# Performance work log

Hardware: AMD Instinct MI355X
Metric: run time of the kernel (lower is better)

## Reference

```python
import jax, jax.numpy as jnp
import numpy as np

N = 50000      # nodes
E = 800000     # edges
CIN = 128
CH = 128
COUT = 64
EPS = 1e-5     # BatchNorm eps


def setup_inputs() -> dict:
    key = jax.random.key(0)
    ks = jax.random.split(key, 16)
    s = 0.1  # weight scale for numerical stability
    return {
        "x": jax.random.normal(ks[0], (N, CIN), jnp.float32),
        "edge_index": jax.random.randint(ks[1], (2, E), 0, N, jnp.int32),
        "edge_weights": jax.random.uniform(ks[2], (E,), jnp.float32),
        "w1": jax.random.normal(ks[3], (CIN, CH), jnp.float32) * s,
        "b1": jnp.zeros((CH,), jnp.float32),
        "bn1_g": jnp.ones((CH,), jnp.float32),
        "bn1_b": jnp.zeros((CH,), jnp.float32),
        "bn1_m": jax.random.normal(ks[4], (CH,), jnp.float32) * 0.1,
        "bn1_v": jax.random.uniform(ks[5], (CH,), jnp.float32) + 0.5,
        "conv_ws": jax.random.normal(ks[6], (2, CH, CH), jnp.float32) * s,
        "conv_bs": jnp.zeros((2, CH), jnp.float32),
        "bns_g": jnp.ones((2, CH), jnp.float32),
        "bns_b": jnp.zeros((2, CH), jnp.float32),
        "bns_m": jax.random.normal(ks[7], (2, CH), jnp.float32) * 0.1,
        "bns_v": jax.random.uniform(ks[8], (2, CH), jnp.float32) + 0.5,
        "lin1_w": jax.random.normal(ks[9], (CH, CH), jnp.float32) * s,
        "lin1_b": jnp.zeros((CH,), jnp.float32),
        "lin2_w": jax.random.normal(ks[10], (CH, COUT), jnp.float32) * s,
        "lin2_b": jnp.zeros((COUT,), jnp.float32),
    }


def _bn(h, g, b, m, v):
    # BatchNorm1d in eval mode: running statistics
    return (h - m) * jax.lax.rsqrt(v + EPS) * g + b


def _gcn(h, w, b, src, dst, norm, n):
    # GCNConv: out[dst] += norm_e * (h @ W)[src]  (self loops already in src/dst)
    h = h @ w
    msg = h[src] * norm[:, None]                 # [E+N, CH]
    return jax.ops.segment_sum(msg, dst, num_segments=n) + b


def reference(x, edge_index, edge_weights, w1, b1, bn1_g, bn1_b, bn1_m, bn1_v,
              conv_ws, conv_bs, bns_g, bns_b, bns_m, bns_v,
              lin1_w, lin1_b, lin2_w, lin2_b):
    n = x.shape[0]
    loop = jnp.arange(n, dtype=edge_index.dtype)
    src = jnp.concatenate([edge_index[0], loop])
    dst = jnp.concatenate([edge_index[1], loop])
    ew = jnp.concatenate([edge_weights, jnp.ones((n,), edge_weights.dtype)])
    # symmetric degree normalization (PyG gcn_norm)
    deg = jax.ops.segment_sum(ew, dst, num_segments=n)
    dis = jnp.where(deg > 0, jax.lax.rsqrt(deg), 0.0)
    norm = dis[src] * ew * dis[dst]

    lrelu = jax.nn.leaky_relu  # slope 0.01, matches F.leaky_relu default
    h = lrelu(_bn(_gcn(x, w1, b1, src, dst, norm, n), bn1_g, bn1_b, bn1_m, bn1_v))
    for i in range(conv_ws.shape[0]):
        h = lrelu(_bn(_gcn(h, conv_ws[i], conv_bs[i], src, dst, norm, n),
                      bns_g[i], bns_b[i], bns_m[i], bns_v[i]) + h)
    h = lrelu(h @ lin1_w + lin1_b)
    # dropout is identity in eval mode
    return h @ lin2_w + lin2_b
```

## Files before the change

kernel.cpp:

```cpp
#include <hip/hip_runtime.h>
#include <hip/hip_bf16.h>


constexpr int   NN    = 50000;
constexpr int   EE    = 800000;
constexpr int   CH    = 128;
constexpr int   SLOTS = 64;
constexpr int   NBUK  = 782;
constexpr int   RCAP  = 2048;
constexpr int   EPB   = 2048;
constexpr float EPS   = 1e-5f;

typedef __attribute__((ext_vector_type(8))) short bf16x8;
typedef __attribute__((ext_vector_type(4))) float f32x4;
typedef unsigned long long u64;
typedef unsigned short u16;

__device__ inline u16 f2bf_rne(float f) {
  unsigned u = __float_as_uint(f);
  unsigned r = u + 0x7fffu + ((u >> 16) & 1u);
  return (u16)(r >> 16);
}
__device__ inline float bf2f(unsigned h16) {
  return __uint_as_float(h16 << 16);
}


__global__ __launch_bounds__(256) void bin_kernel(const int* __restrict__ ei,
                                                  const float* __restrict__ ew,
                                                  unsigned* __restrict__ gcur,
                                                  u64* __restrict__ bins) {
  __shared__ unsigned cnt[NBUK];
  __shared__ unsigned base[NBUK];
  const int tid = threadIdx.x;
  for (int b = tid; b < NBUK; b += 256) cnt[b] = 0;
  __syncthreads();
  const int e0 = blockIdx.x * EPB;
  unsigned pk[8]; u16 bkt[8]; u16 rnk[8]; unsigned char dl[8];
  #pragma unroll
  for (int i = 0; i < 8; i++) {
    int e = e0 + i * 256 + tid;
    if (e < EE) {
      int s = ei[e], d = ei[EE + e];
      float w = ew[e];
      bkt[i] = (u16)(d >> 6);
      dl[i]  = (unsigned char)(d & 63);
      pk[i]  = ((unsigned)f2bf_rne(w) << 16) | (unsigned)s;
      rnk[i] = (u16)atomicAdd(&cnt[bkt[i]], 1u);
    } else bkt[i] = 0xffffu;
  }
  __syncthreads();
  for (int b = tid; b < NBUK; b += 256) {
    unsigned c = cnt[b];
    base[b] = c ? atomicAdd(&gcur[b * 16], c) : 0u;
  }
  __syncthreads();
  #pragma unroll
  for (int i = 0; i < 8; i++) {
    if (bkt[i] == 0xffffu) continue;
    unsigned pos = base[bkt[i]] + rnk[i];
    if (pos < RCAP)
      bins[(size_t)bkt[i] * RCAP + pos] = ((u64)dl[i] << 32) | pk[i];
  }
}


__global__ __launch_bounds__(256) void scatter_kernel(const unsigned* __restrict__ gcur,
                                                      const u64* __restrict__ bins,
                                                      unsigned* __restrict__ ell,
                                                      float* __restrict__ dis) {
  __shared__ unsigned rank[64];
  __shared__ float    wsum[64];
  const int b   = blockIdx.x;
  const int tid = threadIdx.x;
  if (tid < 64) { rank[tid] = 1u; wsum[tid] = 0.f; }
  __syncthreads();
  unsigned cnt = gcur[b * 16];
  if (cnt > RCAP) cnt = RCAP;
  const u64* src = bins + (size_t)b * RCAP;
  for (unsigned i = tid; i < cnt; i += 256) {
    u64 v = src[i];
    unsigned pk = (unsigned)v;
    unsigned dl = (unsigned)(v >> 32);
    unsigned r = atomicAdd(&rank[dl], 1u);
    if (r < SLOTS)
      ell[((size_t)(b * 64 + dl)) * SLOTS + r] = pk;
    atomicAdd(&wsum[dl], bf2f(pk >> 16));
  }
  __syncthreads();
  if (tid < 64) {
    int node = b * 64 + tid;
    if (node < NN) {
      unsigned c = rank[tid];
      if (c > SLOTS) c = SLOTS;
      ell[(size_t)node * SLOTS] = c;
      dis[node] = rsqrtf(1.0f + wsum[tid]);
    }
  }
}

constexpr int NB_WZ = (73728 + 384 + 255) / 256;

__global__ void wswz_kernel(
    const float* __restrict__ w1, const float* __restrict__ bn1_g, const float* __restrict__ bn1_v,
    const float* __restrict__ conv_ws, const float* __restrict__ bns_g, const float* __restrict__ bns_v,
    const float* __restrict__ lin1_w, const float* __restrict__ lin2_w,
    const float* __restrict__ b1, const float* __restrict__ bn1_b, const float* __restrict__ bn1_m,
    const float* __restrict__ conv_bs, const float* __restrict__ bns_b, const float* __restrict__ bns_m,
    u16* __restrict__ w1h, u16* __restrict__ w1l,
    u16* __restrict__ c0h, u16* __restrict__ c0l,
    u16* __restrict__ c1h, u16* __restrict__ c1l,
    u16* __restrict__ l1h, u16* __restrict__ l1l,
    u16* __restrict__ l2h, u16* __restrict__ l2l,
    float* __restrict__ beff)
{
  int idx = blockIdx.x * 256 + threadIdx.x;
  if (idx >= 73728) {
    int r = idx - 73728;
    if (r >= 384) return;
    int l = r >> 7, c = r & 127;
    float bc, gg, bb, mm, vv;
    if (l == 0) { bc = b1[c]; gg = bn1_g[c]; bb = bn1_b[c]; mm = bn1_m[c]; vv = bn1_v[c]; }
    else {
      int o = (l - 1) * 128 + c;
      bc = conv_bs[o]; gg = bns_g[o]; bb = bns_b[o]; mm = bns_m[o]; vv = bns_v[o];
    }
    beff[r] = (bc - mm) * gg * rsqrtf(vv + EPS) + bb;
    return;
  }
  const float* W; const float* g = nullptr; const float* v = nullptr;
  u16 *hi, *lo; int CO = 128; int local;
  if      (idx < 16384) { W = w1;              g = bn1_g;     v = bn1_v;     hi = w1h; lo = w1l; local = idx; }
  else if (idx < 32768) { W = conv_ws;         g = bns_g;     v = bns_v;     hi = c0h; lo = c0l; local = idx - 16384; }
  else if (idx < 49152) { W = conv_ws + 16384; g = bns_g+128; v = bns_v+128; hi = c1h; lo = c1l; local = idx - 32768; }
  else if (idx < 65536) { W = lin1_w;                                        hi = l1h; lo = l1l; local = idx - 49152; }
  else                  { W = lin2_w;                                        hi = l2h; lo = l2l; local = idx - 65536; CO = 64; }
  int k = local / CO, n = local % CO;
  float w = W[local];
  if (g) w *= g[n] * rsqrtf(v[n] + EPS);
  int NCT = CO / 16;
  int kchunk = k >> 5, kin = k & 31, quad = kin >> 3, j = kin & 7;
  int ct = n >> 4, l = (quad << 4) | (n & 15);
  size_t pos = ((size_t)(kchunk * NCT + ct) * 64 + l) * 8 + j;
  u16 h = f2bf_rne(w);
  hi[pos] = h;
  lo[pos] = f2bf_rne(w - bf2f(h));
}

__global__ __launch_bounds__(256) void gemm1_kernel(
    const float* __restrict__ Ain,
    const u16* __restrict__ Whi, const u16* __restrict__ Wlo,
    const float* __restrict__ dis, u16* __restrict__ Cout)
{
  __shared__ float lds[64][CH + 4];
  const int tid  = threadIdx.x;
  const int wave = tid >> 6;
  const int lane = tid & 63;
  const int quad = lane >> 4;
  const int mrow = lane & 15;
  const int row0 = blockIdx.x * 64;

  int arow = row0 + wave * 16 + mrow;
  if (arow >= NN) arow = NN - 1;

  bf16x8 ahi[4], alo[4];
  const float* Ar = Ain + (size_t)arow * CH;
  #pragma unroll
  for (int c = 0; c < 4; c++) {
    int off = c * 32 + quad * 8;
    float4 f0 = *(const float4*)(Ar + off);
    float4 f1 = *(const float4*)(Ar + off + 4);
    float f[8] = {f0.x, f0.y, f0.z, f0.w, f1.x, f1.y, f1.z, f1.w};
    #pragma unroll
    for (int j = 0; j < 8; j++) {
      u16 h = f2bf_rne(f[j]);
      ahi[c][j] = (short)h;
      alo[c][j] = (short)f2bf_rne(f[j] - bf2f(h));
    }
  }

  f32x4 acc[8];
  #pragma unroll
  for (int t = 0; t < 8; t++) acc[t] = (f32x4){0.f, 0.f, 0.f, 0.f};
  #pragma unroll
  for (int c = 0; c < 4; c++) {
    #pragma unroll
    for (int t = 0; t < 8; t++) {
      size_t base = ((size_t)(c * 8 + t) * 64 + lane) * 8;
      bf16x8 bh = *(const bf16x8*)(Whi + base);
      bf16x8 bl = *(const bf16x8*)(Wlo + base);
      acc[t] = __builtin_amdgcn_mfma_f32_16x16x32_bf16(ahi[c], bh, acc[t], 0, 0, 0);
      acc[t] = __builtin_amdgcn_mfma_f32_16x16x32_bf16(alo[c], bh, acc[t], 0, 0, 0);
      acc[t] = __builtin_amdgcn_mfma_f32_16x16x32_bf16(ahi[c], bl, acc[t], 0, 0, 0);
    }
  }

  #pragma unroll
  for (int t = 0; t < 8; t++)
    #pragma unroll
    for (int r = 0; r < 4; r++)
      lds[wave * 16 + quad * 4 + r][t * 16 + mrow] = acc[t][r];
  __syncthreads();

  #pragma unroll
  for (int i = tid; i < 64 * CH / 4; i += 256) {
    int row = (i * 4) / CH;
    int col = (i * 4) % CH;
    int grow = row0 + row;
    if (grow >= NN) continue;
    float rs = dis[grow];
    const float* lp = &lds[row][col];
    u16* cp = (u16*)Cout + (size_t)grow * CH + col;
    unsigned p0 = ((unsigned)f2bf_rne(lp[1] * rs) << 16) | f2bf_rne(lp[0] * rs);
    unsigned p1 = ((unsigned)f2bf_rne(lp[3] * rs) << 16) | f2bf_rne(lp[2] * rs);
    *(uint2*)cp = make_uint2(p0, p1);
  }
}

template<bool RES, bool WH>
__device__ __forceinline__ void gather4_pipe(
    const u16* __restrict__ hwin, const unsigned* __restrict__ ell,
    const float* __restrict__ dis, const float* __restrict__ beff,
    const u16* __restrict__ res, u16* __restrict__ hout,
    unsigned* __restrict__ hsrow,
    int nbase, int lane, int sub, int grp)
{
  auto ndof = [&](int r) { int n = nbase + r; return n < NN ? n : NN - 1; };

  unsigned wcur  = ell[(size_t)ndof(0) * SLOTS + lane];
  unsigned wnext = ell[(size_t)ndof(1) * SLOTS + lane];

  int r = 0, j = 0;
  int cnt = __shfl((int)wcur, 0); if (cnt > SLOTS) cnt = SLOTS;

  float a[8] = {0.f, 0.f, 0.f, 0.f, 0.f, 0.f, 0.f, 0.f};

  unsigned sA[4]; float wA[4]; uint4 hA[4];

  {
    int nd0 = ndof(0);
    #pragma unroll
    for (int q = 0; q < 4; q++) {
      int jj = q * 4 + grp;
      unsigned e = (unsigned)__shfl((int)wcur, jj);
      float wv = (jj == 0) ? 1.0f : bf2f(e >> 16);
      unsigned s = (jj == 0) ? (unsigned)nd0 : (e & 0xffffu);
      if (jj >= cnt) { wv = 0.f; s = (unsigned)nd0; }
      sA[q] = s; wA[q] = wv;
    }
    #pragma unroll
    for (int q = 0; q < 4; q++)
      hA[q] = *(const uint4*)(hwin + (size_t)sA[q] * CH + sub * 8);
  }

  while (true) {
    int jn = j + 16, rn = r;
    const bool cross = (jn >= cnt);
    if (cross) { rn = r + 1; jn = 0; }
    const bool havenext = (rn < 4);

    unsigned sB[4]; float wB[4]; uint4 hB[4];
    int cntN = cnt;
    if (havenext) {
      unsigned wsel = cross ? wnext : wcur;
      if (cross) { cntN = __shfl((int)wnext, 0); if (cntN > SLOTS) cntN = SLOTS; }
      int ndn = ndof(rn);
      #pragma unroll
      for (int q = 0; q < 4; q++) {
        int jj = jn + q * 4 + grp;
        unsigned e = (unsigned)__shfl((int)wsel, jj & 63);
        float wv = (jj == 0) ? 1.0f : bf2f(e >> 16);
        unsigned s = (jj == 0) ? (unsigned)ndn : (e & 0xffffu);
        if (jj >= cntN) { wv = 0.f; s = (unsigned)ndn; }
        sB[q] = s; wB[q] = wv;
      }
      #pragma unroll
      for (int q = 0; q < 4; q++)
        hB[q] = *(const uint4*)(hwin + (size_t)sB[q] * CH + sub * 8);
    }

    #pragma unroll
    for (int q = 0; q < 4; q++) {
      float w = wA[q];
      a[0] = fmaf(w, bf2f(hA[q].x & 0xffffu), a[0]); a[1] = fmaf(w, bf2f(hA[q].x >> 16), a[1]);
      a[2] = fmaf(w, bf2f(hA[q].y & 0xffffu), a[2]); a[3] = fmaf(w, bf2f(hA[q].y >> 16), a[3]);
      a[4] = fmaf(w, bf2f(hA[q].z & 0xffffu), a[4]); a[5] = fmaf(w, bf2f(hA[q].z >> 16), a[5]);
      a[6] = fmaf(w, bf2f(hA[q].w & 0xffffu), a[6]); a[7] = fmaf(w, bf2f(hA[q].w >> 16), a[7]);
    }

    if (cross) {
      #pragma unroll
      for (int k = 0; k < 8; k++) {
        a[k] += __shfl_xor(a[k], 16);
        a[k] += __shfl_xor(a[k], 32);
      }
      int nd = ndof(r), node = nbase + r;
      if (grp == 0) {
        float disd = dis[nd];
        int c = sub * 8;
        float4 be0 = *(const float4*)(beff + c);
        float4 be1 = *(const float4*)(beff + c + 4);
        float y[8];
        y[0] = a[0] * disd + be0.x; y[1] = a[1] * disd + be0.y;
        y[2] = a[2] * disd + be0.z; y[3] = a[3] * disd + be0.w;
        y[4] = a[4] * disd + be1.x; y[5] = a[5] * disd + be1.y;
        y[6] = a[6] * disd + be1.z; y[7] = a[7] * disd + be1.w;
        if constexpr (RES) {
          uint4 rr = *(const uint4*)(res + (size_t)nd * CH + c);
          y[0] += bf2f(rr.x & 0xffffu); y[1] += bf2f(rr.x >> 16);
          y[2] += bf2f(rr.y & 0xffffu); y[3] += bf2f(rr.y >> 16);
          y[4] += bf2f(rr.z & 0xffffu); y[5] += bf2f(rr.z >> 16);
          y[6] += bf2f(rr.w & 0xffffu); y[7] += bf2f(rr.w >> 16);
        }
        #pragma unroll
        for (int k = 0; k < 8; k++) y[k] = y[k] > 0.f ? y[k] : 0.01f * y[k];
        uint4 o;
        o.x = ((unsigned)f2bf_rne(y[1]) << 16) | f2bf_rne(y[0]);
        o.y = ((unsigned)f2bf_rne(y[3]) << 16) | f2bf_rne(y[2]);
        o.z = ((unsigned)f2bf_rne(y[5]) << 16) | f2bf_rne(y[4]);
        o.w = ((unsigned)f2bf_rne(y[7]) << 16) | f2bf_rne(y[6]);
        if constexpr (WH) {
          if (node < NN) *(uint4*)(hout + (size_t)node * CH + c) = o;
        }
        *(uint4*)&hsrow[r * 68 + sub * 4] = o;
      }
      #pragma unroll
      for (int k = 0; k < 8; k++) a[k] = 0.f;
      wcur = wnext;
      if (r + 2 < 4) wnext = ell[(size_t)ndof(r + 2) * SLOTS + lane];
      if (havenext) cnt = cntN;
    }

    if (!havenext) break;
    r = rn; j = jn;
    #pragma unroll
    for (int q = 0; q < 4; q++) { sA[q] = sB[q]; wA[q] = wB[q]; hA[q] = hB[q]; }
  }
}

template<bool RES>
__global__ __launch_bounds__(256, 6) void fuse_kernel(
    const u16* __restrict__ hwin,
    const unsigned* __restrict__ ell, const float* __restrict__ dis,
    const float* __restrict__ beff, const u16* __restrict__ res,
    const u16* __restrict__ Whi, const u16* __restrict__ Wlo,
    u16* __restrict__ hout, u16* __restrict__ hwout)
{
  __shared__ unsigned hs[16][68];
  const int tid  = threadIdx.x;
  const int wave = tid >> 6;
  const int lane = tid & 63;
  const int sub  = lane & 15;
  const int grp  = lane >> 4;
  const int row0 = blockIdx.x * 16;

  gather4_pipe<RES, true>(hwin, ell, dis, beff, res, hout,
                          &hs[wave * 4][0], row0 + wave * 4, lane, sub, grp);
  __syncthreads();

  bf16x8 af[4];
  #pragma unroll
  for (int c = 0; c < 4; c++)
    af[c] = *(const bf16x8*)&hs[sub][c * 16 + grp * 4];

  f32x4 acc[2];
  #pragma unroll
  for (int t = 0; t < 2; t++) acc[t] = (f32x4){0.f, 0.f, 0.f, 0.f};
  #pragma unroll
  for (int c = 0; c < 4; c++) {
    #pragma unroll
    for (int t = 0; t < 2; t++) {
      size_t base = ((size_t)(c * 8 + wave * 2 + t) * 64 + lane) * 8;
      bf16x8 bh = *(const bf16x8*)(Whi + base);
      bf16x8 bl = *(const bf16x8*)(Wlo + base);
      acc[t] = __builtin_amdgcn_mfma_f32_16x16x32_bf16(af[c], bh, acc[t], 0, 0, 0);
      acc[t] = __builtin_amdgcn_mfma_f32_16x16x32_bf16(af[c], bl, acc[t], 0, 0, 0);
    }
  }

  #pragma unroll
  for (int r = 0; r < 4; r++) {
    int grow = row0 + grp * 4 + r;
    if (grow >= NN) continue;
    float rs = dis[grow];
    #pragma unroll
    for (int t = 0; t < 2; t++)
      hwout[(size_t)grow * CH + wave * 32 + t * 16 + sub] = f2bf_rne(acc[t][r] * rs);
  }
}

__global__ __launch_bounds__(256, 6) void fuse_last_kernel(
    const u16* __restrict__ hwin,
    const unsigned* __restrict__ ell, const float* __restrict__ dis,
    const float* __restrict__ beff, const u16* __restrict__ res,
    const u16* __restrict__ l1h, const u16* __restrict__ l1l,
    const float* __restrict__ b1,
    const u16* __restrict__ l2h, const u16* __restrict__ l2l,
    const float* __restrict__ b2, float* __restrict__ out)
{
  __shared__ unsigned hs[16][68];
  __shared__ float    fs[16][132];
  const int tid  = threadIdx.x;
  const int wave = tid >> 6;
  const int lane = tid & 63;
  const int sub  = lane & 15;
  const int grp  = lane >> 4;
  const int row0 = blockIdx.x * 16;

  gather4_pipe<true, false>(hwin, ell, dis, beff, res, nullptr,
                            &hs[wave * 4][0], row0 + wave * 4, lane, sub, grp);
  __syncthreads();

  bf16x8 af[4];
  #pragma unroll
  for (int c = 0; c < 4; c++)
    af[c] = *(const bf16x8*)&hs[sub][c * 16 + grp * 4];

  f32x4 acc[2];
  #pragma unroll
  for (int t = 0; t < 2; t++) acc[t] = (f32x4){0.f, 0.f, 0.f, 0.f};
  #pragma unroll
  for (int c = 0; c < 4; c++) {
    #pragma unroll
    for (int t = 0; t < 2; t++) {
      size_t base = ((size_t)(c * 8 + wave * 2 + t) * 64 + lane) * 8;
      bf16x8 bh = *(const bf16x8*)(l1h + base);
      bf16x8 bl = *(const bf16x8*)(l1l + base);
      acc[t] = __builtin_amdgcn_mfma_f32_16x16x32_bf16(af[c], bh, acc[t], 0, 0, 0);
      acc[t] = __builtin_amdgcn_mfma_f32_16x16x32_bf16(af[c], bl, acc[t], 0, 0, 0);
    }
  }
  #pragma unroll
  for (int t = 0; t < 2; t++) {
    int col = wave * 32 + t * 16 + sub;
    float bb = b1[col];
    #pragma unroll
    for (int r = 0; r < 4; r++) {
      float x = acc[t][r] + bb;
      x = x > 0.f ? x : 0.01f * x;
      fs[grp * 4 + r][col] = x;
    }
  }
  __syncthreads();

  f32x4 acc2 = (f32x4){0.f, 0.f, 0.f, 0.f};
  #pragma unroll
  for (int c = 0; c < 4; c++) {
    bf16x8 ahi, alo;
    const float* lp = &fs[sub][c * 32 + grp * 8];
    float4 f0 = *(const float4*)lp;
    float4 f1 = *(const float4*)(lp + 4);
    float f[8] = {f0.x, f0.y, f0.z, f0.w, f1.x, f1.y, f1.z, f1.w};
    #pragma unroll
    for (int j = 0; j < 8; j++) {
      u16 h = f2bf_rne(f[j]);
      ahi[j] = (short)h;
      alo[j] = (short)f2bf_rne(f[j] - bf2f(h));
    }
    size_t base = ((size_t)(c * 4 + wave) * 64 + lane) * 8;
    bf16x8 bh = *(const bf16x8*)(l2h + base);
    bf16x8 bl = *(const bf16x8*)(l2l + base);
    acc2 = __builtin_amdgcn_mfma_f32_16x16x32_bf16(ahi, bh, acc2, 0, 0, 0);
    acc2 = __builtin_amdgcn_mfma_f32_16x16x32_bf16(alo, bh, acc2, 0, 0, 0);
    acc2 = __builtin_amdgcn_mfma_f32_16x16x32_bf16(ahi, bl, acc2, 0, 0, 0);
  }
  {
    float bb = b2[wave * 16 + sub];
    #pragma unroll
    for (int r = 0; r < 4; r++) {
      int grow = row0 + grp * 4 + r;
      if (grow < NN)
        out[(size_t)grow * 64 + wave * 16 + sub] = acc2[r] + bb;
    }
  }
}


extern "C" void kernel_launch(void* const* d_in, const int* in_sizes, int n_in,
                              void* d_out, int out_size, void* d_ws, size_t ws_size,
                              hipStream_t stream) {
  const float* x       = (const float*)d_in[0];
  const int*   ei      = (const int*)  d_in[1];
  const float* ew      = (const float*)d_in[2];
  const float* w1      = (const float*)d_in[3];
  const float* b1      = (const float*)d_in[4];
  const float* bn1_g   = (const float*)d_in[5];
  const float* bn1_b   = (const float*)d_in[6];
  const float* bn1_m   = (const float*)d_in[7];
  const float* bn1_v   = (const float*)d_in[8];
  const float* conv_ws = (const float*)d_in[9];
  const float* conv_bs = (const float*)d_in[10];
  const float* bns_g   = (const float*)d_in[11];
  const float* bns_b   = (const float*)d_in[12];
  const float* bns_m   = (const float*)d_in[13];
  const float* bns_v   = (const float*)d_in[14];
  const float* lin1_w  = (const float*)d_in[15];
  const float* lin1_b  = (const float*)d_in[16];
  const float* lin2_w  = (const float*)d_in[17];
  const float* lin2_b  = (const float*)d_in[18];
  float* out = (float*)d_out;

  size_t off = 0;
  auto alloc = [&](size_t elems) -> void* {
    void* p = (char*)d_ws + off * 4;
    off += (elems + 3) & ~(size_t)3;
    return p;
  };
  unsigned* gcur = (unsigned*)alloc(NBUK * 16);
  u64*      bins = (u64*)     alloc((size_t)NBUK * RCAP * 2);
  unsigned* ell  = (unsigned*)alloc((size_t)NN * SLOTS);
  float*    dis  = (float*)   alloc(NN);
  float*    beff = (float*)   alloc(3 * CH);
  u16*      hwa  = (u16*)     alloc((size_t)NN * CH / 2);
  u16*      hwb  = (u16*)     alloc((size_t)NN * CH / 2);
  u16*      h1   = (u16*)     alloc((size_t)NN * CH / 2);
  u16*      h2   = (u16*)     alloc((size_t)NN * CH / 2);
  u16* w1h = (u16*)alloc(CH * CH / 2); u16* w1l = (u16*)alloc(CH * CH / 2);
  u16* c0h = (u16*)alloc(CH * CH / 2); u16* c0l = (u16*)alloc(CH * CH / 2);
  u16* c1h = (u16*)alloc(CH * CH / 2); u16* c1l = (u16*)alloc(CH * CH / 2);
  u16* l1h = (u16*)alloc(CH * CH / 2); u16* l1l = (u16*)alloc(CH * CH / 2);
  u16* l2h = (u16*)alloc(CH * 64 / 2); u16* l2l = (u16*)alloc(CH * 64 / 2);

  const int nb_bin  = (EE + EPB - 1) / EPB;
  const int nb_gemm = (NN + 63) / 64;
  const int nb_fuse = (NN + 15) / 16;
  dim3 B(256);

  hipMemsetAsync(gcur, 0, NBUK * 16 * sizeof(unsigned), stream);
  bin_kernel    <<<nb_bin, B, 0, stream>>>(ei, ew, gcur, bins);
  scatter_kernel<<<NBUK,   B, 0, stream>>>(gcur, bins, ell, dis);

  wswz_kernel<<<NB_WZ, B, 0, stream>>>(w1, bn1_g, bn1_v, conv_ws, bns_g, bns_v,
      lin1_w, lin2_w, b1, bn1_b, bn1_m, conv_bs, bns_b, bns_m,
      w1h, w1l, c0h, c0l, c1h, c1l, l1h, l1l, l2h, l2l, beff);

  gemm1_kernel<<<nb_gemm, B, 0, stream>>>(x, w1h, w1l, dis, hwa);

  fuse_kernel<false><<<nb_fuse, B, 0, stream>>>(hwa, ell, dis, beff, nullptr,
      c0h, c0l, h1, hwb);

  fuse_kernel<true><<<nb_fuse, B, 0, stream>>>(hwb, ell, dis, beff + CH, h1,
      c1h, c1l, h2, hwa);

  fuse_last_kernel<<<nb_fuse, B, 0, stream>>>(hwa, ell, dis, beff + 2 * CH, h2,
      l1h, l1l, lin1_b, l2h, l2l, lin2_b, out);
}
```

Baseline: 368.4 us.

## Assign one node per 16-lane group in gather instead of sequential node pipeline

The per-wave gather now gives each 16-lane group its own destination node and walks that node's neighbour list in chunks of eight loads, replacing the software-pipelined loop that processed four nodes one after another with cross-group shuffle reductions. This removes the per-node cross-lane reductions and serial node switching, and issues more independent row loads per iteration. In exchange, the loop runs to the maximum degree among the four nodes, so groups with shorter lists issue wasted masked loads of the node's own row. The explicit software prefetch of the next batch is also dropped, and the NN bounds clamp is gone.

```diff
diff --git a/kernel.cpp b/kernel.cpp
--- a/kernel.cpp
+++ b/kernel.cpp
@@ -218,124 +218,78 @@
 }
 
 template<bool RES, bool WH>
-__device__ __forceinline__ void gather4_pipe(
+__device__ __forceinline__ void gather4_grp(
     const u16* __restrict__ hwin, const unsigned* __restrict__ ell,
     const float* __restrict__ dis, const float* __restrict__ beff,
     const u16* __restrict__ res, u16* __restrict__ hout,
-    unsigned* __restrict__ hsrow,
+    unsigned* __restrict__ hsbase,
     int nbase, int lane, int sub, int grp)
 {
-  auto ndof = [&](int r) { int n = nbase + r; return n < NN ? n : NN - 1; };
-
-  unsigned wcur  = ell[(size_t)ndof(0) * SLOTS + lane];
-  unsigned wnext = ell[(size_t)ndof(1) * SLOTS + lane];
-
-  int r = 0, j = 0;
-  int cnt = __shfl((int)wcur, 0); if (cnt > SLOTS) cnt = SLOTS;
+  const int node = nbase + grp;
+  const size_t ebase = (size_t)node * SLOTS + sub;
+  unsigned w0 = ell[ebase];
+  unsigned w1 = ell[ebase + 16];
+  unsigned w2 = ell[ebase + 32];
+  unsigned w3 = ell[ebase + 48];
+
+  int cme = __shfl((int)w0, grp << 4); if (cme > SLOTS) cme = SLOTS;
+  int c0 = __shfl((int)w0, 0),  c1 = __shfl((int)w0, 16);
+  int c2 = __shfl((int)w0, 32), c3 = __shfl((int)w0, 48);
+  int cmax = max(max(c0, c1), max(c2, c3)); if (cmax > SLOTS) cmax = SLOTS;
 
   float a[8] = {0.f, 0.f, 0.f, 0.f, 0.f, 0.f, 0.f, 0.f};
-
-  unsigned sA[4]; float wA[4]; uint4 hA[4];
-
-  {
-    int nd0 = ndof(0);
-    #pragma unroll
-    for (int q = 0; q < 4; q++) {
-      int jj = q * 4 + grp;
-      unsigned e = (unsigned)__shfl((int)wcur, jj);
+  const u16* hrow = hwin + sub * 8;
+
+  for (int j = 0; j < cmax; j += 8) {
+    uint4 hQ[8]; float wQ[8];
+    #pragma unroll
+    for (int u = 0; u < 8; u++) {
+      int jj = j + u;
+      int k = jj >> 4;
+      unsigned wsel = k == 0 ? w0 : (k == 1 ? w1 : (k == 2 ? w2 : w3));
+      unsigned e = (unsigned)__shfl((int)wsel, (grp << 4) | (jj & 15));
       float wv = (jj == 0) ? 1.0f : bf2f(e >> 16);
-      unsigned s = (jj == 0) ? (unsigned)nd0 : (e & 0xffffu);
-      if (jj >= cnt) { wv = 0.f; s = (unsigned)nd0; }
-      sA[q] = s; wA[q] = wv;
-    }
-    #pragma unroll
-    for (int q = 0; q < 4; q++)
-      hA[q] = *(const uint4*)(hwin + (size_t)sA[q] * CH + sub * 8);
-  }
-
-  while (true) {
-    int jn = j + 16, rn = r;
-    const bool cross = (jn >= cnt);
-    if (cross) { rn = r + 1; jn = 0; }
-    const bool havenext = (rn < 4);
-
-    unsigned sB[4]; float wB[4]; uint4 hB[4];
-    int cntN = cnt;
-    if (havenext) {
-      unsigned wsel = cross ? wnext : wcur;
-      if (cross) { cntN = __shfl((int)wnext, 0); if (cntN > SLOTS) cntN = SLOTS; }
-      int ndn = ndof(rn);
-      #pragma unroll
-      for (int q = 0; q < 4; q++) {
-        int jj = jn + q * 4 + grp;
-        unsigned e = (unsigned)__shfl((int)wsel, jj & 63);
-        float wv = (jj == 0) ? 1.0f : bf2f(e >> 16);
-        unsigned s = (jj == 0) ? (unsigned)ndn : (e & 0xffffu);
-        if (jj >= cntN) { wv = 0.f; s = (unsigned)ndn; }
-        sB[q] = s; wB[q] = wv;
-      }
-      #pragma unroll
-      for (int q = 0; q < 4; q++)
-        hB[q] = *(const uint4*)(hwin + (size_t)sB[q] * CH + sub * 8);
-    }
-
-    #pragma unroll
-    for (int q = 0; q < 4; q++) {
-      float w = wA[q];
-      a[0] = fmaf(w, bf2f(hA[q].x & 0xffffu), a[0]); a[1] = fmaf(w, bf2f(hA[q].x >> 16), a[1]);
-      a[2] = fmaf(w, bf2f(hA[q].y & 0xffffu), a[2]); a[3] = fmaf(w, bf2f(hA[q].y >> 16), a[3]);
-      a[4] = fmaf(w, bf2f(hA[q].z & 0xffffu), a[4]); a[5] = fmaf(w, bf2f(hA[q].z >> 16), a[5]);
-      a[6] = fmaf(w, bf2f(hA[q].w & 0xffffu), a[6]); a[7] = fmaf(w, bf2f(hA[q].w >> 16), a[7]);
-    }
-
-    if (cross) {
-      #pragma unroll
-      for (int k = 0; k < 8; k++) {
-        a[k] += __shfl_xor(a[k], 16);
-        a[k] += __shfl_xor(a[k], 32);
-      }
-      int nd = ndof(r), node = nbase + r;
-      if (grp == 0) {
-        float disd = dis[nd];
-        int c = sub * 8;
-        float4 be0 = *(const float4*)(beff + c);
-        float4 be1 = *(const float4*)(beff + c + 4);
-        float y[8];
-        y[0] = a[0] * disd + be0.x; y[1] = a[1] * disd + be0.y;
-        y[2] = a[2] * disd + be0.z; y[3] = a[3] * disd + be0.w;
-        y[4] = a[4] * disd + be1.x; y[5] = a[5] * disd + be1.y;
-        y[6] = a[6] * disd + be1.z; y[7] = a[7] * disd + be1.w;
-        if constexpr (RES) {
-          uint4 rr = *(const uint4*)(res + (size_t)nd * CH + c);
-          y[0] += bf2f(rr.x & 0xffffu); y[1] += bf2f(rr.x >> 16);
-          y[2] += bf2f(rr.y & 0xffffu); y[3] += bf2f(rr.y >> 16);
-          y[4] += bf2f(rr.z & 0xffffu); y[5] += bf2f(rr.z >> 16);
-          y[6] += bf2f(rr.w & 0xffffu); y[7] += bf2f(rr.w >> 16);
-        }
-        #pragma unroll
-        for (int k = 0; k < 8; k++) y[k] = y[k] > 0.f ? y[k] : 0.01f * y[k];
-        uint4 o;
-        o.x = ((unsigned)f2bf_rne(y[1]) << 16) | f2bf_rne(y[0]);
-        o.y = ((unsigned)f2bf_rne(y[3]) << 16) | f2bf_rne(y[2]);
-        o.z = ((unsigned)f2bf_rne(y[5]) << 16) | f2bf_rne(y[4]);
-        o.w = ((unsigned)f2bf_rne(y[7]) << 16) | f2bf_rne(y[6]);
-        if constexpr (WH) {
-          if (node < NN) *(uint4*)(hout + (size_t)node * CH + c) = o;
-        }
-        *(uint4*)&hsrow[r * 68 + sub * 4] = o;
-      }
-      #pragma unroll
-      for (int k = 0; k < 8; k++) a[k] = 0.f;
-      wcur = wnext;
-      if (r + 2 < 4) wnext = ell[(size_t)ndof(r + 2) * SLOTS + lane];
-      if (havenext) cnt = cntN;
-    }
-
-    if (!havenext) break;
-    r = rn; j = jn;
-    #pragma unroll
-    for (int q = 0; q < 4; q++) { sA[q] = sB[q]; wA[q] = wB[q]; hA[q] = hB[q]; }
-  }
+      unsigned s = (jj == 0) ? (unsigned)node : (e & 0xffffu);
+      if (jj >= cme) { wv = 0.f; s = (unsigned)node; }
+      wQ[u] = wv;
+      hQ[u] = *(const uint4*)(hrow + (size_t)s * CH);
+    }
+    #pragma unroll
+    for (int u = 0; u < 8; u++) {
+      float w = wQ[u];
+      a[0] = fmaf(w, bf2f(hQ[u].x & 0xffffu), a[0]); a[1] = fmaf(w, bf2f(hQ[u].x >> 16), a[1]);
+      a[2] = fmaf(w, bf2f(hQ[u].y & 0xffffu), a[2]); a[3] = fmaf(w, bf2f(hQ[u].y >> 16), a[3]);
+      a[4] = fmaf(w, bf2f(hQ[u].z & 0xffffu), a[4]); a[5] = fmaf(w, bf2f(hQ[u].z >> 16), a[5]);
+      a[6] = fmaf(w, bf2f(hQ[u].w & 0xffffu), a[6]); a[7] = fmaf(w, bf2f(hQ[u].w >> 16), a[7]);
+    }
+  }
+
+  float disd = dis[node];
+  int c = sub * 8;
+  float4 be0 = *(const float4*)(beff + c);
+  float4 be1 = *(const float4*)(beff + c + 4);
+  float y[8];
+  y[0] = a[0] * disd + be0.x; y[1] = a[1] * disd + be0.y;
+  y[2] = a[2] * disd + be0.z; y[3] = a[3] * disd + be0.w;
+  y[4] = a[4] * disd + be1.x; y[5] = a[5] * disd + be1.y;
+  y[6] = a[6] * disd + be1.z; y[7] = a[7] * disd + be1.w;
+  if constexpr (RES) {
+    uint4 rr = *(const uint4*)(res + (size_t)node * CH + c);
+    y[0] += bf2f(rr.x & 0xffffu); y[1] += bf2f(rr.x >> 16);
+    y[2] += bf2f(rr.y & 0xffffu); y[3] += bf2f(rr.y >> 16);
+    y[4] += bf2f(rr.z & 0xffffu); y[5] += bf2f(rr.z >> 16);
+    y[6] += bf2f(rr.w & 0xffffu); y[7] += bf2f(rr.w >> 16);
+  }
+  #pragma unroll
+  for (int k = 0; k < 8; k++) y[k] = y[k] > 0.f ? y[k] : 0.01f * y[k];
+  uint4 o;
+  o.x = ((unsigned)f2bf_rne(y[1]) << 16) | f2bf_rne(y[0]);
+  o.y = ((unsigned)f2bf_rne(y[3]) << 16) | f2bf_rne(y[2]);
+  o.z = ((unsigned)f2bf_rne(y[5]) << 16) | f2bf_rne(y[4]);
+  o.w = ((unsigned)f2bf_rne(y[7]) << 16) | f2bf_rne(y[6]);
+  if constexpr (WH)
+    *(uint4*)(hout + (size_t)node * CH + c) = o;
+  *(uint4*)&hsbase[grp * 68 + sub * 4] = o;
 }
 
 template<bool RES>
@@ -354,8 +308,8 @@
   const int grp  = lane >> 4;
   const int row0 = blockIdx.x * 16;
 
-  gather4_pipe<RES, true>(hwin, ell, dis, beff, res, hout,
-                          &hs[wave * 4][0], row0 + wave * 4, lane, sub, grp);
+  gather4_grp<RES, true>(hwin, ell, dis, beff, res, hout,
+                         &hs[wave * 4][0], row0 + wave * 4, lane, sub, grp);
   __syncthreads();
 
   bf16x8 af[4];
@@ -407,8 +361,8 @@
   const int grp  = lane >> 4;
   const int row0 = blockIdx.x * 16;
 
-  gather4_pipe<true, false>(hwin, ell, dis, beff, res, nullptr,
-                            &hs[wave * 4][0], row0 + wave * 4, lane, sub, grp);
+  gather4_grp<true, false>(hwin, ell, dis, beff, res, nullptr,
+                           &hs[wave * 4][0], row0 + wave * 4, lane, sub, grp);
   __syncthreads();
 
   bf16x8 af[4];
```

Result: faster. 333.7 us (-9.4%).
